# Kernel optimization log

Hardware: AMD Instinct MI355X
Metric: run time of the kernel (lower is better)

Reference implementation:

```python
import jax, jax.numpy as jnp
import numpy as np

N_HEAD, D_K = 8, 16

def _ln(x, g, b):
    m = jnp.mean(x, -1, keepdims=True)
    v = jnp.var(x, -1, keepdims=True)
    return (x - m) * jax.lax.rsqrt(v + 1e-5) * g + b

def _enc_layer(x, wq, bq, wk, bk, wv, bv, wo, bo, g1, be1, cw1, cb1, cw2, cb2, g2, be2):
    B, L, D = x.shape
    q = (x @ wq + bq).reshape(B, L, N_HEAD, D_K)
    k = (x @ wk + bk).reshape(B, L, N_HEAD, D_K)
    v = (x @ wv + bv).reshape(B, L, N_HEAD, D_K)
    attn = jnp.einsum('blhd,bmhd->bhlm', q, k) / jnp.sqrt(jnp.float32(D_K))
    attn = jax.nn.softmax(attn, axis=-1)
    o = jnp.einsum('bhlm,bmhd->blhd', attn, v).reshape(B, L, -1)
    x = _ln(o @ wo + bo + x, g1, be1)          # post-LN residual (MHA)
    h = jax.nn.relu(x @ cw1 + cb1)             # 1x1 conv == linear
    return _ln(h @ cw2 + cb2 + x, g2, be2)     # post-LN residual (FFN)

def setup_inputs() -> dict:
    key = jax.random.key(0)
    ks = jax.random.split(key, 20)
    N, D, NNZ = 100000, 128, 2000000
    B, L, NL, DI = 32, 256, 2, 512
    s = 0.02
    inp = {}
    inp['ego'] = jax.random.normal(ks[0], (N, D), jnp.float32)
    inp['vals'] = jax.random.uniform(ks[1], (NNZ,), jnp.float32) / 20.0  # ~normalized adj values
    inp['W1'] = jax.random.normal(ks[2], (D, D), jnp.float32) * s
    inp['b1'] = jnp.zeros((D,), jnp.float32)
    inp['W2'] = jax.random.normal(ks[3], (D, D), jnp.float32) * s
    inp['b2'] = jnp.zeros((D,), jnp.float32)
    inp['enc_in'] = jax.random.normal(ks[4], (B, L, D), jnp.float32)
    inp['wq'] = jax.random.normal(ks[5], (NL, D, D), jnp.float32) * s
    inp['bq'] = jnp.zeros((NL, D), jnp.float32)
    inp['wk'] = jax.random.normal(ks[6], (NL, D, D), jnp.float32) * s
    inp['bk'] = jnp.zeros((NL, D), jnp.float32)
    inp['wv'] = jax.random.normal(ks[7], (NL, D, D), jnp.float32) * s
    inp['bv'] = jnp.zeros((NL, D), jnp.float32)
    inp['wo'] = jax.random.normal(ks[8], (NL, D, D), jnp.float32) * s
    inp['bo'] = jnp.zeros((NL, D), jnp.float32)
    inp['ln1_g'] = jnp.ones((NL, D), jnp.float32)
    inp['ln1_b'] = jnp.zeros((NL, D), jnp.float32)
    inp['cw1'] = jax.random.normal(ks[9], (NL, D, DI), jnp.float32) * s
    inp['cb1'] = jnp.zeros((NL, DI), jnp.float32)
    inp['cw2'] = jax.random.normal(ks[10], (NL, DI, D), jnp.float32) * s
    inp['cb2'] = jnp.zeros((NL, D), jnp.float32)
    inp['ln2_g'] = jnp.ones((NL, D), jnp.float32)
    inp['ln2_b'] = jnp.zeros((NL, D), jnp.float32)
    inp['rows'] = jnp.sort(jax.random.randint(ks[11], (NNZ,), 0, N, jnp.int32))
    inp['cols'] = jax.random.randint(ks[12], (NNZ,), 0, N, jnp.int32)
    return inp

def reference(ego, vals, W1, b1, W2, b2, enc_in, wq, bq, wk, bk, wv, bv, wo, bo,
              ln1_g, ln1_b, cw1, cb1, cw2, cb2, ln2_g, ln2_b, rows, cols):
    N = ego.shape[0]
    # sparse A_in @ ego  (COO SpMM via gather + segment_sum)
    side = jax.ops.segment_sum(vals[:, None] * ego[cols], rows, num_segments=N)
    # bi-interaction aggregator (dropout=identity in eval)
    sum_emb = jax.nn.leaky_relu((ego + side) @ W1 + b1)
    bi_emb = jax.nn.leaky_relu((ego * side) @ W2 + b2)
    agg = sum_emb + bi_emb
    # transformer encoder over edge sequences
    x = enc_in
    for i in range(wq.shape[0]):
        x = _enc_layer(x, wq[i], bq[i], wk[i], bk[i], wv[i], bv[i], wo[i], bo[i],
                       ln1_g[i], ln1_b[i], cw1[i], cb1[i], cw2[i], cb2[i], ln2_g[i], ln2_b[i])
    return (agg, x)
```

## Files before the change

### kernel.cpp

```cpp
#include <hip/hip_runtime.h>

typedef __attribute__((ext_vector_type(8))) short bf16x8;
typedef __attribute__((ext_vector_type(4))) float f32x4;

__device__ __forceinline__ unsigned short f2b(float f) {
    union { float f; unsigned int i; } u; u.f = f;
    return (unsigned short)((u.i + 0x7FFFu + ((u.i >> 16) & 1u)) >> 16);
}
__device__ __forceinline__ unsigned int packbf2(float a, float b) {
    return (unsigned int)f2b(a) | ((unsigned int)f2b(b) << 16);
}

__device__ __forceinline__ void spmm_block(
    const unsigned int* __restrict__ egob, const float* __restrict__ vals,
    const int* __restrict__ rows, const int* __restrict__ cols,
    float* __restrict__ side, int nnz, int blk)
{
    int tid = threadIdx.x;
    int wave = tid >> 6, lane = tid & 63;
    int e0 = blk * 256 + wave * 64;
    if (e0 >= nnz) return;

    int idx = e0 + lane;
    int last = nnz - 1;
    bool ok = idx < nnz;
    int safe = ok ? idx : last;
    int my_row = rows[safe];
    int my_col = cols[safe];
    float my_val = ok ? vals[safe] : 0.f;

    unsigned int pre[16];
    #pragma unroll
    for (int j = 0; j < 16; ++j) {
        unsigned int c = (unsigned int)__builtin_amdgcn_readlane(my_col, j);
        pre[j] = *(egob + ((size_t)c << 6) + lane);
    }

    float ax = 0.f, ay = 0.f;
    int cur = __builtin_amdgcn_readlane(my_row, 0);
    #pragma unroll
    for (int e = 0; e < 64; ++e) {
        int r = __builtin_amdgcn_readlane(my_row, e);
        float vv = __int_as_float(__builtin_amdgcn_readlane(__float_as_int(my_val), e));
        unsigned int u = pre[e & 15];
        if (e < 48) {
            unsigned int c = (unsigned int)__builtin_amdgcn_readlane(my_col, e + 16);
            pre[e & 15] = *(egob + ((size_t)c << 6) + lane);
        }
        if (r != cur) {
            atomicAdd(&side[(size_t)cur * 128 + lane * 2], ax);
            atomicAdd(&side[(size_t)cur * 128 + lane * 2 + 1], ay);
            ax = 0.f; ay = 0.f; cur = r;
        }
        ax = fmaf(vv, __uint_as_float(u << 16), ax);
        ay = fmaf(vv, __uint_as_float(u & 0xFFFF0000u), ay);
    }
    atomicAdd(&side[(size_t)cur * 128 + lane * 2], ax);
    atomicAdd(&side[(size_t)cur * 128 + lane * 2 + 1], ay);
}

#define LDAB 40
#define LDBI 72
#define LDKV 16

__device__ __forceinline__ void gemm2_core(
    const float* __restrict__ A, const float* __restrict__ W,
    const float* __restrict__ bias, const float* __restrict__ R,
    const float* __restrict__ g, const float* __restrict__ bta,
    float* __restrict__ C, int M, int N, int K, int act,
    int bm, int bn, unsigned short* As, unsigned short* Bs,
    float* redS, float* redSS)
{
    int tid = threadIdx.x, wave = tid >> 6, lane = tid & 63;
    int lm = lane & 15, quad = lane >> 4;
    int wm = wave >> 1, wn = wave & 1;

    f32x4 acc[2][4];
    #pragma unroll
    for (int i = 0; i < 2; ++i)
        #pragma unroll
        for (int j = 0; j < 4; ++j) acc[i][j] = (f32x4)(0.f);

    for (int k0 = 0; k0 < K; k0 += 32) {
        {
            int m = tid >> 2, kc = (tid & 3) * 8;
            const float* p = A + (size_t)(bm + m) * K + k0 + kc;
            float4 a0 = *(const float4*)p, a1 = *(const float4*)(p + 4);
            uint4 pk;
            pk.x = packbf2(a0.x, a0.y); pk.y = packbf2(a0.z, a0.w);
            pk.z = packbf2(a1.x, a1.y); pk.w = packbf2(a1.z, a1.w);
            *(uint4*)&As[m * LDAB + kc] = pk;
        }
        {
            int nn = tid & 127, kh = (tid >> 7) * 16;
            const float* p = W + (size_t)(k0 + kh) * N + bn + nn;
            float w[16];
            #pragma unroll
            for (int j = 0; j < 16; ++j) w[j] = p[(size_t)j * N];
            uint4 pk;
            pk.x = packbf2(w[0], w[1]);  pk.y = packbf2(w[2], w[3]);
            pk.z = packbf2(w[4], w[5]);  pk.w = packbf2(w[6], w[7]);
            *(uint4*)&Bs[nn * LDAB + kh] = pk;
            pk.x = packbf2(w[8], w[9]);  pk.y = packbf2(w[10], w[11]);
            pk.z = packbf2(w[12], w[13]); pk.w = packbf2(w[14], w[15]);
            *(uint4*)&Bs[nn * LDAB + kh + 8] = pk;
        }
        __syncthreads();
        bf16x8 af[2], bfr[4];
        #pragma unroll
        for (int mi = 0; mi < 2; ++mi)
            af[mi] = *(bf16x8*)&As[(wm * 32 + mi * 16 + lm) * LDAB + quad * 8];
        #pragma unroll
        for (int ni = 0; ni < 4; ++ni)
            bfr[ni] = *(bf16x8*)&Bs[(wn * 64 + ni * 16 + lm) * LDAB + quad * 8];
        #pragma unroll
        for (int mi = 0; mi < 2; ++mi)
            #pragma unroll
            for (int ni = 0; ni < 4; ++ni)
                acc[mi][ni] = __builtin_amdgcn_mfma_f32_16x16x32_bf16(
                    af[mi], bfr[ni], acc[mi][ni], 0, 0, 0);
        __syncthreads();
    }

    #pragma unroll
    for (int mi = 0; mi < 2; ++mi) {
        #pragma unroll
        for (int r = 0; r < 4; ++r) {
            int row = bm + wm * 32 + mi * 16 + quad * 4 + r;
            #pragma unroll
            for (int ni = 0; ni < 4; ++ni) {
                int col = bn + wn * 64 + ni * 16 + lm;
                float v = acc[mi][ni][r] + bias[col];
                if (R) v += R[(size_t)row * N + col];
                if (act) v = fmaxf(v, 0.f);
                acc[mi][ni][r] = v;
            }
        }
    }

    if (g) {
        #pragma unroll
        for (int mi = 0; mi < 2; ++mi) {
            #pragma unroll
            for (int r = 0; r < 4; ++r) {
                float s = 0.f, ss = 0.f;
                #pragma unroll
                for (int ni = 0; ni < 4; ++ni) {
                    float v = acc[mi][ni][r];
                    s += v; ss = fmaf(v, v, ss);
                }
                #pragma unroll
                for (int off = 1; off < 16; off <<= 1) {
                    s  += __shfl_xor(s, off, 64);
                    ss += __shfl_xor(ss, off, 64);
                }
                if (lm == 0) {
                    int lr = wm * 32 + mi * 16 + quad * 4 + r;
                    redS[wn * 64 + lr] = s;
                    redSS[wn * 64 + lr] = ss;
                }
            }
        }
        __syncthreads();
        #pragma unroll
        for (int mi = 0; mi < 2; ++mi) {
            #pragma unroll
            for (int r = 0; r < 4; ++r) {
                int lr = wm * 32 + mi * 16 + quad * 4 + r;
                int row = bm + lr;
                float s = redS[lr] + redS[64 + lr];
                float ss = redSS[lr] + redSS[64 + lr];
                float mean = s * (1.f / 128.f);
                float var = ss * (1.f / 128.f) - mean * mean;
                float rstd = rsqrtf(var + 1e-5f);
                #pragma unroll
                for (int ni = 0; ni < 4; ++ni) {
                    int col = wn * 64 + ni * 16 + lm;
                    float y = (acc[mi][ni][r] - mean) * rstd * g[col] + bta[col];
                    C[(size_t)row * 128 + col] = y;
                }
            }
        }
    } else {
        #pragma unroll
        for (int mi = 0; mi < 2; ++mi) {
            #pragma unroll
            for (int r = 0; r < 4; ++r) {
                int row = bm + wm * 32 + mi * 16 + quad * 4 + r;
                #pragma unroll
                for (int ni = 0; ni < 4; ++ni) {
                    int col = bn + wn * 64 + ni * 16 + lm;
                    C[(size_t)row * N + col] = acc[mi][ni][r];
                }
            }
        }
    }
}

__device__ __forceinline__ void bi_core3(
    const float* __restrict__ ego, const float* __restrict__ side,
    const unsigned short* __restrict__ W1t, const unsigned short* __restrict__ W2t,
    const float* __restrict__ b1, const float* __restrict__ b2,
    float* __restrict__ out, int M, int bm,
    unsigned short* Us, unsigned short* Ms)
{
    int tid = threadIdx.x, wave = tid >> 6, lane = tid & 63;
    int lm = lane & 15, quad = lane >> 4;
    int wm = wave >> 1, wn = wave & 1;

    f32x4 acc1[2][4], acc2[2][4];
    #pragma unroll
    for (int i = 0; i < 2; ++i)
        #pragma unroll
        for (int j = 0; j < 4; ++j) { acc1[i][j] = (f32x4)(0.f); acc2[i][j] = (f32x4)(0.f); }

    #pragma unroll
    for (int h = 0; h < 2; ++h) {
        int k0 = h * 64;
        if (h) __syncthreads();
        {
            int m = tid >> 2, kc = (tid & 3) * 16;
            int gm = bm + m;
            float e[16], s[16];
            if (gm < M) {
                const float* pe = ego + (size_t)gm * 128 + k0 + kc;
                const float* ps = side + (size_t)gm * 128 + k0 + kc;
                #pragma unroll
                for (int j = 0; j < 4; ++j) {
                    float4 ev = *(const float4*)(pe + j * 4);
                    float4 sv = *(const float4*)(ps + j * 4);
                    e[j*4+0] = ev.x; e[j*4+1] = ev.y; e[j*4+2] = ev.z; e[j*4+3] = ev.w;
                    s[j*4+0] = sv.x; s[j*4+1] = sv.y; s[j*4+2] = sv.z; s[j*4+3] = sv.w;
                }
            } else {
                #pragma unroll
                for (int j = 0; j < 16; ++j) { e[j] = 0.f; s[j] = 0.f; }
            }
            #pragma unroll
            for (int j = 0; j < 2; ++j) {
                int b0 = j * 8;
                uint4 pu, pv;
                pu.x = packbf2(e[b0+0]+s[b0+0], e[b0+1]+s[b0+1]);
                pu.y = packbf2(e[b0+2]+s[b0+2], e[b0+3]+s[b0+3]);
                pu.z = packbf2(e[b0+4]+s[b0+4], e[b0+5]+s[b0+5]);
                pu.w = packbf2(e[b0+6]+s[b0+6], e[b0+7]+s[b0+7]);
                pv.x = packbf2(e[b0+0]*s[b0+0], e[b0+1]*s[b0+1]);
                pv.y = packbf2(e[b0+2]*s[b0+2], e[b0+3]*s[b0+3]);
                pv.z = packbf2(e[b0+4]*s[b0+4], e[b0+5]*s[b0+5]);
                pv.w = packbf2(e[b0+6]*s[b0+6], e[b0+7]*s[b0+7]);
                *(uint4*)&Us[m * LDBI + kc + b0] = pu;
                *(uint4*)&Ms[m * LDBI + kc + b0] = pv;
            }
        }
        __syncthreads();
        #pragma unroll
        for (int ks = 0; ks < 2; ++ks) {
            bf16x8 au[2], am[2], bf1[4], bf2[4];
            #pragma unroll
            for (int mi = 0; mi < 2; ++mi) {
                int off = (wm * 32 + mi * 16 + lm) * LDBI + ks * 32 + quad * 8;
                au[mi] = *(bf16x8*)&Us[off];
                am[mi] = *(bf16x8*)&Ms[off];
            }
            #pragma unroll
            for (int ni = 0; ni < 4; ++ni) {
                size_t n = (size_t)(wn * 64 + ni * 16 + lm);
                size_t koff = n * 128 + k0 + ks * 32 + quad * 8;
                bf1[ni] = *(const bf16x8*)(W1t + koff);
                bf2[ni] = *(const bf16x8*)(W2t + koff);
            }
            #pragma unroll
            for (int mi = 0; mi < 2; ++mi)
                #pragma unroll
                for (int ni = 0; ni < 4; ++ni) {
                    acc1[mi][ni] = __builtin_amdgcn_mfma_f32_16x16x32_bf16(
                        au[mi], bf1[ni], acc1[mi][ni], 0, 0, 0);
                    acc2[mi][ni] = __builtin_amdgcn_mfma_f32_16x16x32_bf16(
                        am[mi], bf2[ni], acc2[mi][ni], 0, 0, 0);
                }
        }
    }
    #pragma unroll
    for (int mi = 0; mi < 2; ++mi) {
        #pragma unroll
        for (int r = 0; r < 4; ++r) {
            int row = bm + wm * 32 + mi * 16 + quad * 4 + r;
            if (row < M) {
                #pragma unroll
                for (int ni = 0; ni < 4; ++ni) {
                    int col = wn * 64 + ni * 16 + lm;
                    float v1 = acc1[mi][ni][r] + b1[col];
                    v1 = v1 > 0.f ? v1 : 0.01f * v1;
                    float v2 = acc2[mi][ni][r] + b2[col];
                    v2 = v2 > 0.f ? v2 : 0.01f * v2;
                    out[(size_t)row * 128 + col] = v1 + v2;
                }
            }
        }
    }
}

__device__ __forceinline__ void attn_block(
    const float* __restrict__ q, const float* __restrict__ k,
    const float* __restrict__ v, float* __restrict__ o, int NH,
    int blk, float* Ks, float* Vs)
{
    const int L = 256, DK = 16;
    int bh = blk >> 2, qq = blk & 3;
    int b = bh / NH, h = bh % NH;
    int tid = threadIdx.x;
    int qi = tid >> 2, seg = tid & 3;

    int lq = qq * 64 + qi;
    size_t qbase = ((size_t)(b * L + lq) * NH + h) * DK;
    float qr[16];
    #pragma unroll
    for (int d4 = 0; d4 < 4; ++d4) {
        float4 t = *(const float4*)(q + qbase + d4 * 4);
        qr[d4*4+0] = t.x * 0.25f; qr[d4*4+1] = t.y * 0.25f;
        qr[d4*4+2] = t.z * 0.25f; qr[d4*4+3] = t.w * 0.25f;
    }
    float acc[16];
    #pragma unroll
    for (int d = 0; d < 16; ++d) acc[d] = 0.f;
    float mmax = -1e30f, ssum = 0.f;

    for (int c0 = 0; c0 < L; c0 += 128) {
        __syncthreads();
        for (int i = tid; i < 128 * 4; i += 256) {
            int ll = i >> 2, d4 = (i & 3) * 4;
            size_t gg = ((size_t)(b * L + c0 + ll) * NH + h) * DK + d4;
            *(float4*)&Ks[ll * LDKV + d4] = *(const float4*)(k + gg);
            *(float4*)&Vs[ll * LDKV + d4] = *(const float4*)(v + gg);
        }
        __syncthreads();

        for (int i = 0; i < 32; ++i) {
            int kk = (i << 2) | seg;
            const float* kr = &Ks[kk * LDKV];
            float dot = 0.f;
            #pragma unroll
            for (int d4 = 0; d4 < 4; ++d4) {
                float4 kv = *(const float4*)&kr[d4 * 4];
                dot = fmaf(qr[d4*4+0], kv.x, dot);
                dot = fmaf(qr[d4*4+1], kv.y, dot);
                dot = fmaf(qr[d4*4+2], kv.z, dot);
                dot = fmaf(qr[d4*4+3], kv.w, dot);
            }
            if (dot > mmax) {
                float alpha = __expf(mmax - dot);
                ssum *= alpha;
                #pragma unroll
                for (int d = 0; d < 16; ++d) acc[d] *= alpha;
                mmax = dot;
            }
            float p = __expf(dot - mmax);
            ssum += p;
            const float* vr = &Vs[kk * LDKV];
            #pragma unroll
            for (int d4 = 0; d4 < 4; ++d4) {
                float4 vv = *(const float4*)&vr[d4 * 4];
                acc[d4*4+0] = fmaf(p, vv.x, acc[d4*4+0]);
                acc[d4*4+1] = fmaf(p, vv.y, acc[d4*4+1]);
                acc[d4*4+2] = fmaf(p, vv.z, acc[d4*4+2]);
                acc[d4*4+3] = fmaf(p, vv.w, acc[d4*4+3]);
            }
        }
    }

    float m1 = fmaxf(mmax, __shfl_xor(mmax, 1, 64));
    float m2 = fmaxf(m1, __shfl_xor(m1, 2, 64));
    float f = __expf(mmax - m2);
    float sl = ssum * f;
    sl += __shfl_xor(sl, 1, 64);
    sl += __shfl_xor(sl, 2, 64);
    #pragma unroll
    for (int d = 0; d < 16; ++d) {
        float a = acc[d] * f;
        a += __shfl_xor(a, 1, 64);
        a += __shfl_xor(a, 2, 64);
        acc[d] = a;
    }
    if (seg == 0) {
        float inv = 1.f / sl;
        #pragma unroll
        for (int d4 = 0; d4 < 4; ++d4) {
            float4 t;
            t.x = acc[d4*4+0] * inv; t.y = acc[d4*4+1] * inv;
            t.z = acc[d4*4+2] * inv; t.w = acc[d4*4+3] * inv;
            *(float4*)(o + qbase + d4 * 4) = t;
        }
    }
}


__global__ __launch_bounds__(256) void qkv2_pre(
    const float* __restrict__ A,
    const float* __restrict__ wq, const float* __restrict__ wk, const float* __restrict__ wv,
    const float* __restrict__ bq, const float* __restrict__ bk, const float* __restrict__ bv,
    float* __restrict__ Q, float* __restrict__ Ko, float* __restrict__ V, int M, int encGy,
    float* __restrict__ side, int Nn,
    const float* __restrict__ ego, unsigned int* __restrict__ egob,
    const float* __restrict__ W1, const float* __restrict__ W2,
    unsigned short* __restrict__ W1t, unsigned short* __restrict__ W2t,
    int encN, int ZB, int CB, int WTB)
{
    __shared__ unsigned short As[64 * LDAB];
    __shared__ unsigned short Bs[128 * LDAB];
    __shared__ float redS[128], redSS[128];
    int gid = blockIdx.x;
    int tid = threadIdx.x;
    if (gid >= encN) {
        int j = gid - encN;
        if (j < ZB) {
            size_t n4 = (size_t)Nn * 32;
            float4 z = make_float4(0.f, 0.f, 0.f, 0.f);
            for (size_t i = (size_t)j * 256 + tid; i < n4; i += (size_t)ZB * 256)
                ((float4*)side)[i] = z;
        } else if (j < ZB + CB) {
            int c = j - ZB;
            size_t n4 = (size_t)Nn * 32;
            for (size_t i = (size_t)c * 256 + tid; i < n4; i += (size_t)CB * 256) {
                float4 a = *(const float4*)(ego + i * 4);
                uint2 p;
                p.x = packbf2(a.x, a.y);
                p.y = packbf2(a.z, a.w);
                *(uint2*)(egob + i * 2) = p;
            }
        } else {
            int c = j - ZB - CB;
            for (int ch = c * 256 + tid; ch < 4096; ch += WTB * 256) {
                int w = ch >> 11, rem = ch & 2047;
                int n = rem >> 4, k8 = rem & 15;
                const float* src = w ? W2 : W1;
                unsigned short* dst = w ? W2t : W1t;
                float t[8];
                #pragma unroll
                for (int jj = 0; jj < 8; ++jj)
                    t[jj] = src[(size_t)(k8 * 8 + jj) * 128 + n];
                uint4 pk;
                pk.x = packbf2(t[0], t[1]); pk.y = packbf2(t[2], t[3]);
                pk.z = packbf2(t[4], t[5]); pk.w = packbf2(t[6], t[7]);
                *(uint4*)&dst[(size_t)n * 128 + k8 * 8] = pk;
            }
        }
        return;
    }
    int sel = gid / encGy, by = gid % encGy;
    const float* W = (sel == 0) ? wq : (sel == 1) ? wk : wv;
    const float* b = (sel == 0) ? bq : (sel == 1) ? bk : bv;
    float* C = (sel == 0) ? Q : (sel == 1) ? Ko : V;
    gemm2_core(A, W, b, nullptr, nullptr, nullptr, C, M, 128, 128, 0,
               by * 64, 0, As, Bs, redS, redSS);
}

__global__ __launch_bounds__(256) void qkv2_spmm(
    const float* __restrict__ A,
    const float* __restrict__ wq, const float* __restrict__ wk, const float* __restrict__ wv,
    const float* __restrict__ bq, const float* __restrict__ bk, const float* __restrict__ bv,
    float* __restrict__ Q, float* __restrict__ Ko, float* __restrict__ V, int M, int encGy,
    const unsigned int* __restrict__ egob, const float* __restrict__ vals,
    const int* __restrict__ rows, const int* __restrict__ cols,
    float* __restrict__ side, int nnz, int spmmBase, int encN)
{
    __shared__ unsigned short As[64 * LDAB];
    __shared__ unsigned short Bs[128 * LDAB];
    __shared__ float redS[128], redSS[128];
    int gid = blockIdx.x;
    if (gid >= encN) {
        spmm_block(egob, vals, rows, cols, side, nnz, spmmBase + gid - encN);
        return;
    }
    int sel = gid / encGy, by = gid % encGy;
    const float* W = (sel == 0) ? wq : (sel == 1) ? wk : wv;
    const float* b = (sel == 0) ? bq : (sel == 1) ? bk : bv;
    float* C = (sel == 0) ? Q : (sel == 1) ? Ko : V;
    gemm2_core(A, W, b, nullptr, nullptr, nullptr, C, M, 128, 128, 0,
               by * 64, 0, As, Bs, redS, redSS);
}

__global__ __launch_bounds__(256) void gemm2_spmm(
    const float* __restrict__ A, const float* __restrict__ W,
    const float* __restrict__ bias, const float* __restrict__ R,
    const float* __restrict__ g, const float* __restrict__ bta,
    float* __restrict__ C, int M, int N, int K, int act, int encGy,
    const unsigned int* __restrict__ egob, const float* __restrict__ vals,
    const int* __restrict__ rows, const int* __restrict__ cols,
    float* __restrict__ side, int nnz, int spmmBase, int encN)
{
    __shared__ unsigned short As[64 * LDAB];
    __shared__ unsigned short Bs[128 * LDAB];
    __shared__ float redS[128], redSS[128];
    int gid = blockIdx.x;
    if (gid >= encN) {
        spmm_block(egob, vals, rows, cols, side, nnz, spmmBase + gid - encN);
        return;
    }
    int bx = gid / encGy, by = gid % encGy;
    gemm2_core(A, W, bias, R, g, bta, C, M, N, K, act,
               by * 64, bx * 128, As, Bs, redS, redSS);
}

__global__ __launch_bounds__(256) void gemm2_bi3(
    const float* __restrict__ A, const float* __restrict__ W,
    const float* __restrict__ bias, const float* __restrict__ R,
    const float* __restrict__ g, const float* __restrict__ bta,
    float* __restrict__ C, int M, int N, int K, int act, int encGy, int encN,
    const float* __restrict__ ego, const float* __restrict__ side,
    const unsigned short* __restrict__ W1t, const unsigned short* __restrict__ W2t,
    const float* __restrict__ b1, const float* __restrict__ b2,
    float* __restrict__ out, int Mbi, int biBase)
{
    __shared__ char smem[18432];
    int gid = blockIdx.x;
    if (gid < encN) {
        unsigned short* As = (unsigned short*)smem;
        unsigned short* Bs = (unsigned short*)(smem + 5120);
        float* redS  = (float*)(smem + 15360);
        float* redSS = (float*)(smem + 15360 + 512);
        int bx = gid / encGy, by = gid % encGy;
        gemm2_core(A, W, bias, R, g, bta, C, M, N, K, act,
                   by * 64, bx * 128, As, Bs, redS, redSS);
    } else {
        int bb = biBase + (gid - encN);
        unsigned short* Us = (unsigned short*)smem;
        unsigned short* Ms = (unsigned short*)(smem + 9216);
        bi_core3(ego, side, W1t, W2t, b1, b2, out, Mbi, bb * 64, Us, Ms);
    }
}

__global__ __launch_bounds__(256) void attn_spmm(
    const float* __restrict__ q, const float* __restrict__ k,
    const float* __restrict__ v, float* __restrict__ o, int NH,
    const unsigned int* __restrict__ egob, const float* __restrict__ vals,
    const int* __restrict__ rows, const int* __restrict__ cols,
    float* __restrict__ side, int nnz, int spmmBase, int encN)
{
    __shared__ float Ks[128 * LDKV];
    __shared__ float Vs[128 * LDKV];
    int gid = blockIdx.x;
    if (gid >= encN) {
        spmm_block(egob, vals, rows, cols, side, nnz, spmmBase + gid - encN);
        return;
    }
    attn_block(q, k, v, o, NH, gid, Ks, Vs);
}

extern "C" void kernel_launch(void* const* d_in, const int* in_sizes, int n_in,
                              void* d_out, int out_size, void* d_ws, size_t ws_size,
                              hipStream_t stream) {
    const float* ego    = (const float*)d_in[0];
    const float* vals   = (const float*)d_in[1];
    const float* W1     = (const float*)d_in[2];
    const float* b1     = (const float*)d_in[3];
    const float* W2     = (const float*)d_in[4];
    const float* b2     = (const float*)d_in[5];
    const float* enc_in = (const float*)d_in[6];
    const float* wq  = (const float*)d_in[7];
    const float* bq  = (const float*)d_in[8];
    const float* wk  = (const float*)d_in[9];
    const float* bk  = (const float*)d_in[10];
    const float* wv  = (const float*)d_in[11];
    const float* bv  = (const float*)d_in[12];
    const float* wo  = (const float*)d_in[13];
    const float* bo  = (const float*)d_in[14];
    const float* ln1_g = (const float*)d_in[15];
    const float* ln1_b = (const float*)d_in[16];
    const float* cw1 = (const float*)d_in[17];
    const float* cb1 = (const float*)d_in[18];
    const float* cw2 = (const float*)d_in[19];
    const float* cb2 = (const float*)d_in[20];
    const float* ln2_g = (const float*)d_in[21];
    const float* ln2_b = (const float*)d_in[22];
    const int* rows = (const int*)d_in[23];
    const int* cols = (const int*)d_in[24];

    const int D = 128, DI = 512, NH = 8, L = 256;
    const int Nn   = in_sizes[0] / D;
    const int nnz  = in_sizes[1];
    const int NL   = in_sizes[7] / (D * D);
    const int Menc = in_sizes[6] / D;
    const int Bb   = Menc / L;

    float* ws = (float*)d_ws;
    size_t off = 0;
    float* side = ws + off; off += (size_t)Nn * D;
    float* Qb = ws + off; off += (size_t)Menc * D;
    float* Kb = ws + off; off += (size_t)Menc * D;
    float* Vb = ws + off; off += (size_t)Menc * D;
    float* Ob = ws + off; off += (size_t)Menc * D;
    float* XA = ws + off; off += (size_t)Menc * D;
    float* XB = ws + off; off += (size_t)Menc * D;
    float* Hb = ws + off; off += (size_t)Menc * DI;
    unsigned int* egob = (unsigned int*)(ws + off); off += (size_t)Nn * (D / 2);
    unsigned short* W1t = (unsigned short*)(ws + off); off += (size_t)D * D / 2;
    unsigned short* W2t = (unsigned short*)(ws + off); off += (size_t)D * D / 2;

    float* outAgg = (float*)d_out;
    float* outX   = (float*)d_out + (size_t)Nn * D;

    const int spmmBlocks = (nnz + 255) / 256;
    const int nSpmmStages = 5 * NL - 3;
    const int perS = (spmmBlocks + nSpmmStages - 1) / nSpmmStages;
    const int biTiles = (Nn + 63) / 64;
    const int perB = (biTiles + 1) / 2;
    const int biStart = 5 * NL - 1;
    const int encGy = Menc / 64;
    const int ZB = 512, CB = 1024, WTB = 16;
    int sidx = 0, sci = 0, bci = 0;

    const float* x = enc_in;
    for (int i = 0; i < NL; ++i) {
        const size_t wOff = (size_t)i * D * D;
        int base, cnt;
        #define SPMM_CHUNK base = sci * perS; cnt = spmmBlocks - base; \
                           if (cnt < 0) cnt = 0; if (cnt > perS) cnt = perS; sci++
        #define BI_CHUNK   base = bci * perB; cnt = biTiles - base; \
                           if (cnt < 0) cnt = 0; if (cnt > perB) cnt = perB; bci++

        sidx++;
        if (sidx == 1) {
            qkv2_pre<<<3 * encGy + ZB + CB + WTB, 256, 0, stream>>>(
                x, wq + wOff, wk + wOff, wv + wOff,
                bq + (size_t)i * D, bk + (size_t)i * D, bv + (size_t)i * D,
                Qb, Kb, Vb, Menc, encGy,
                side, Nn, ego, egob, W1, W2, W1t, W2t, 3 * encGy, ZB, CB, WTB);
        } else {
            SPMM_CHUNK;
            qkv2_spmm<<<3 * encGy + cnt, 256, 0, stream>>>(
                x, wq + wOff, wk + wOff, wv + wOff,
                bq + (size_t)i * D, bk + (size_t)i * D, bv + (size_t)i * D,
                Qb, Kb, Vb, Menc, encGy,
                egob, vals, rows, cols, side, nnz, base, 3 * encGy);
        }

        sidx++;
        SPMM_CHUNK;
        attn_spmm<<<Bb * NH * 4 + cnt, 256, 0, stream>>>(
            Qb, Kb, Vb, Ob, NH,
            egob, vals, rows, cols, side, nnz, base, Bb * NH * 4);

        sidx++;
        SPMM_CHUNK;
        gemm2_spmm<<<encGy + cnt, 256, 0, stream>>>(
            Ob, wo + wOff, bo + (size_t)i * D, x,
            ln1_g + (size_t)i * D, ln1_b + (size_t)i * D, XA, Menc, D, D, 0, encGy,
            egob, vals, rows, cols, side, nnz, base, encGy);

        sidx++;
        if (sidx >= biStart) {
            BI_CHUNK;
            gemm2_bi3<<<4 * encGy + cnt, 256, 0, stream>>>(
                XA, cw1 + (size_t)i * D * DI, cb1 + (size_t)i * DI, nullptr,
                nullptr, nullptr, Hb, Menc, DI, D, 1, encGy, 4 * encGy,
                ego, side, W1t, W2t, b1, b2, outAgg, Nn, base);
        } else {
            SPMM_CHUNK;
            gemm2_spmm<<<4 * encGy + cnt, 256, 0, stream>>>(
                XA, cw1 + (size_t)i * D * DI, cb1 + (size_t)i * DI, nullptr,
                nullptr, nullptr, Hb, Menc, DI, D, 1, encGy,
                egob, vals, rows, cols, side, nnz, base, 4 * encGy);
        }

        sidx++;
        float* dst = (i == NL - 1) ? outX : XB;
        if (sidx >= biStart) {
            BI_CHUNK;
            gemm2_bi3<<<encGy + cnt, 256, 0, stream>>>(
                Hb, cw2 + (size_t)i * DI * D, cb2 + (size_t)i * D, XA,
                ln2_g + (size_t)i * D, ln2_b + (size_t)i * D, dst, Menc, D, DI, 0,
                encGy, encGy,
                ego, side, W1t, W2t, b1, b2, outAgg, Nn, base);
        } else {
            SPMM_CHUNK;
            gemm2_spmm<<<encGy + cnt, 256, 0, stream>>>(
                Hb, cw2 + (size_t)i * DI * D, cb2 + (size_t)i * D, XA,
                ln2_g + (size_t)i * D, ln2_b + (size_t)i * D, dst, Menc, D, DI, 0, encGy,
                egob, vals, rows, cols, side, nnz, base, encGy);
        }
        #undef SPMM_CHUNK
        #undef BI_CHUNK
        x = XB;
    }
}
```

Baseline: 453.1 us.

## Place side-work blocks first in fused grids and stage full K in bi-interaction tile

Every fused kernel now numbers its SpMM, zero/convert and bi-interaction blocks before the encoder GEMM/attention blocks, so the long irregular work is dispatched first and the short dense tiles fill in behind it. The bi-interaction core now stages all 128 K columns of the (ego+side) and (ego*side) bf16 tiles in shared memory at once. That drops the second staging pass and one barrier, but raises shared memory for that kernel from 18 KB to 34 KB, which may lower occupancy for the GEMM blocks sharing it.

After: 500.2 us. 10.4% more time.

```diff
diff --git a/kernel.cpp b/kernel.cpp
--- a/kernel.cpp
+++ b/kernel.cpp
@@ -60,7 +60,7 @@
 }
 
 #define LDAB 40
-#define LDBI 72
+#define LDBI2 136
 #define LDKV 16
 
 __device__ __forceinline__ void gemm2_core(
@@ -197,7 +197,7 @@
     }
 }
 
-__device__ __forceinline__ void bi_core3(
+__device__ __forceinline__ void bi_core4(
     const float* __restrict__ ego, const float* __restrict__ side,
     const unsigned short* __restrict__ W1t, const unsigned short* __restrict__ W2t,
     const float* __restrict__ b1, const float* __restrict__ b2,
@@ -214,71 +214,67 @@
         #pragma unroll
         for (int j = 0; j < 4; ++j) { acc1[i][j] = (f32x4)(0.f); acc2[i][j] = (f32x4)(0.f); }
 
-    #pragma unroll
-    for (int h = 0; h < 2; ++h) {
-        int k0 = h * 64;
-        if (h) __syncthreads();
-        {
-            int m = tid >> 2, kc = (tid & 3) * 16;
-            int gm = bm + m;
-            float e[16], s[16];
-            if (gm < M) {
-                const float* pe = ego + (size_t)gm * 128 + k0 + kc;
-                const float* ps = side + (size_t)gm * 128 + k0 + kc;
-                #pragma unroll
-                for (int j = 0; j < 4; ++j) {
-                    float4 ev = *(const float4*)(pe + j * 4);
-                    float4 sv = *(const float4*)(ps + j * 4);
-                    e[j*4+0] = ev.x; e[j*4+1] = ev.y; e[j*4+2] = ev.z; e[j*4+3] = ev.w;
-                    s[j*4+0] = sv.x; s[j*4+1] = sv.y; s[j*4+2] = sv.z; s[j*4+3] = sv.w;
-                }
-            } else {
-                #pragma unroll
-                for (int j = 0; j < 16; ++j) { e[j] = 0.f; s[j] = 0.f; }
-            }
-            #pragma unroll
-            for (int j = 0; j < 2; ++j) {
-                int b0 = j * 8;
-                uint4 pu, pv;
-                pu.x = packbf2(e[b0+0]+s[b0+0], e[b0+1]+s[b0+1]);
-                pu.y = packbf2(e[b0+2]+s[b0+2], e[b0+3]+s[b0+3]);
-                pu.z = packbf2(e[b0+4]+s[b0+4], e[b0+5]+s[b0+5]);
-                pu.w = packbf2(e[b0+6]+s[b0+6], e[b0+7]+s[b0+7]);
-                pv.x = packbf2(e[b0+0]*s[b0+0], e[b0+1]*s[b0+1]);
-                pv.y = packbf2(e[b0+2]*s[b0+2], e[b0+3]*s[b0+3]);
-                pv.z = packbf2(e[b0+4]*s[b0+4], e[b0+5]*s[b0+5]);
-                pv.w = packbf2(e[b0+6]*s[b0+6], e[b0+7]*s[b0+7]);
-                *(uint4*)&Us[m * LDBI + kc + b0] = pu;
-                *(uint4*)&Ms[m * LDBI + kc + b0] = pv;
-            }
-        }
-        __syncthreads();
-        #pragma unroll
-        for (int ks = 0; ks < 2; ++ks) {
-            bf16x8 au[2], am[2], bf1[4], bf2[4];
-            #pragma unroll
-            for (int mi = 0; mi < 2; ++mi) {
-                int off = (wm * 32 + mi * 16 + lm) * LDBI + ks * 32 + quad * 8;
-                au[mi] = *(bf16x8*)&Us[off];
-                am[mi] = *(bf16x8*)&Ms[off];
-            }
+    {
+        int m = tid >> 2, kc = (tid & 3) * 32;
+        int gm = bm + m;
+        float e[32], s[32];
+        if (gm < M) {
+            const float* pe = ego + (size_t)gm * 128 + kc;
+            const float* ps = side + (size_t)gm * 128 + kc;
+            #pragma unroll
+            for (int j = 0; j < 8; ++j) {
+                float4 ev = *(const float4*)(pe + j * 4);
+                float4 sv = *(const float4*)(ps + j * 4);
+                e[j*4+0] = ev.x; e[j*4+1] = ev.y; e[j*4+2] = ev.z; e[j*4+3] = ev.w;
+                s[j*4+0] = sv.x; s[j*4+1] = sv.y; s[j*4+2] = sv.z; s[j*4+3] = sv.w;
+            }
+        } else {
+            #pragma unroll
+            for (int j = 0; j < 32; ++j) { e[j] = 0.f; s[j] = 0.f; }
+        }
+        #pragma unroll
+        for (int j = 0; j < 4; ++j) {
+            int b0 = j * 8;
+            uint4 pu, pv;
+            pu.x = packbf2(e[b0+0]+s[b0+0], e[b0+1]+s[b0+1]);
+            pu.y = packbf2(e[b0+2]+s[b0+2], e[b0+3]+s[b0+3]);
+            pu.z = packbf2(e[b0+4]+s[b0+4], e[b0+5]+s[b0+5]);
+            pu.w = packbf2(e[b0+6]+s[b0+6], e[b0+7]+s[b0+7]);
+            pv.x = packbf2(e[b0+0]*s[b0+0], e[b0+1]*s[b0+1]);
+            pv.y = packbf2(e[b0+2]*s[b0+2], e[b0+3]*s[b0+3]);
+            pv.z = packbf2(e[b0+4]*s[b0+4], e[b0+5]*s[b0+5]);
+            pv.w = packbf2(e[b0+6]*s[b0+6], e[b0+7]*s[b0+7]);
+            *(uint4*)&Us[m * LDBI2 + kc + b0] = pu;
+            *(uint4*)&Ms[m * LDBI2 + kc + b0] = pv;
+        }
+    }
+    __syncthreads();
+
+    #pragma unroll
+    for (int ks = 0; ks < 4; ++ks) {
+        bf16x8 au[2], am[2], bf1[4], bf2[4];
+        #pragma unroll
+        for (int mi = 0; mi < 2; ++mi) {
+            int off = (wm * 32 + mi * 16 + lm) * LDBI2 + ks * 32 + quad * 8;
+            au[mi] = *(bf16x8*)&Us[off];
+            am[mi] = *(bf16x8*)&Ms[off];
+        }
+        #pragma unroll
+        for (int ni = 0; ni < 4; ++ni) {
+            size_t n = (size_t)(wn * 64 + ni * 16 + lm);
+            size_t koff = n * 128 + ks * 32 + quad * 8;
+            bf1[ni] = *(const bf16x8*)(W1t + koff);
+            bf2[ni] = *(const bf16x8*)(W2t + koff);
+        }
+        #pragma unroll
+        for (int mi = 0; mi < 2; ++mi)
             #pragma unroll
             for (int ni = 0; ni < 4; ++ni) {
-                size_t n = (size_t)(wn * 64 + ni * 16 + lm);
-                size_t koff = n * 128 + k0 + ks * 32 + quad * 8;
-                bf1[ni] = *(const bf16x8*)(W1t + koff);
-                bf2[ni] = *(const bf16x8*)(W2t + koff);
-            }
-            #pragma unroll
-            for (int mi = 0; mi < 2; ++mi)
-                #pragma unroll
-                for (int ni = 0; ni < 4; ++ni) {
-                    acc1[mi][ni] = __builtin_amdgcn_mfma_f32_16x16x32_bf16(
-                        au[mi], bf1[ni], acc1[mi][ni], 0, 0, 0);
-                    acc2[mi][ni] = __builtin_amdgcn_mfma_f32_16x16x32_bf16(
-                        am[mi], bf2[ni], acc2[mi][ni], 0, 0, 0);
-                }
-        }
+                acc1[mi][ni] = __builtin_amdgcn_mfma_f32_16x16x32_bf16(
+                    au[mi], bf1[ni], acc1[mi][ni], 0, 0, 0);
+                acc2[mi][ni] = __builtin_amdgcn_mfma_f32_16x16x32_bf16(
+                    am[mi], bf2[ni], acc2[mi][ni], 0, 0, 0);
+            }
     }
     #pragma unroll
     for (int mi = 0; mi < 2; ++mi) {
@@ -403,15 +399,15 @@
     const float* __restrict__ ego, unsigned int* __restrict__ egob,
     const float* __restrict__ W1, const float* __restrict__ W2,
     unsigned short* __restrict__ W1t, unsigned short* __restrict__ W2t,
-    int encN, int ZB, int CB, int WTB)
+    int ZB, int CB, int WTB)
 {
     __shared__ unsigned short As[64 * LDAB];
     __shared__ unsigned short Bs[128 * LDAB];
     __shared__ float redS[128], redSS[128];
     int gid = blockIdx.x;
     int tid = threadIdx.x;
-    if (gid >= encN) {
-        int j = gid - encN;
+    if (gid < ZB + CB + WTB) {
+        int j = gid;
         if (j < ZB) {
             size_t n4 = (size_t)Nn * 32;
             float4 z = make_float4(0.f, 0.f, 0.f, 0.f);
@@ -446,7 +442,8 @@
         }
         return;
     }
-    int sel = gid / encGy, by = gid % encGy;
+    int egid = gid - (ZB + CB + WTB);
+    int sel = egid / encGy, by = egid % encGy;
     const float* W = (sel == 0) ? wq : (sel == 1) ? wk : wv;
     const float* b = (sel == 0) ? bq : (sel == 1) ? bk : bv;
     float* C = (sel == 0) ? Q : (sel == 1) ? Ko : V;
@@ -461,17 +458,18 @@
     float* __restrict__ Q, float* __restrict__ Ko, float* __restrict__ V, int M, int encGy,
     const unsigned int* __restrict__ egob, const float* __restrict__ vals,
     const int* __restrict__ rows, const int* __restrict__ cols,
-    float* __restrict__ side, int nnz, int spmmBase, int encN)
+    float* __restrict__ side, int nnz, int spmmBase, int sideCnt)
 {
     __shared__ unsigned short As[64 * LDAB];
     __shared__ unsigned short Bs[128 * LDAB];
     __shared__ float redS[128], redSS[128];
     int gid = blockIdx.x;
-    if (gid >= encN) {
-        spmm_block(egob, vals, rows, cols, side, nnz, spmmBase + gid - encN);
+    if (gid < sideCnt) {
+        spmm_block(egob, vals, rows, cols, side, nnz, spmmBase + gid);
         return;
     }
-    int sel = gid / encGy, by = gid % encGy;
+    int egid = gid - sideCnt;
+    int sel = egid / encGy, by = egid % encGy;
     const float* W = (sel == 0) ? wq : (sel == 1) ? wk : wv;
     const float* b = (sel == 0) ? bq : (sel == 1) ? bk : bv;
     float* C = (sel == 0) ? Q : (sel == 1) ? Ko : V;
@@ -486,46 +484,49 @@
     float* __restrict__ C, int M, int N, int K, int act, int encGy,
     const unsigned int* __restrict__ egob, const float* __restrict__ vals,
     const int* __restrict__ rows, const int* __restrict__ cols,
-    float* __restrict__ side, int nnz, int spmmBase, int encN)
+    float* __restrict__ side, int nnz, int spmmBase, int sideCnt)
 {
     __shared__ unsigned short As[64 * LDAB];
     __shared__ unsigned short Bs[128 * LDAB];
     __shared__ float redS[128], redSS[128];
     int gid = blockIdx.x;
-    if (gid >= encN) {
-        spmm_block(egob, vals, rows, cols, side, nnz, spmmBase + gid - encN);
+    if (gid < sideCnt) {
+        spmm_block(egob, vals, rows, cols, side, nnz, spmmBase + gid);
         return;
     }
-    int bx = gid / encGy, by = gid % encGy;
+    int egid = gid - sideCnt;
+    int bx = egid / encGy, by = egid % encGy;
     gemm2_core(A, W, bias, R, g, bta, C, M, N, K, act,
                by * 64, bx * 128, As, Bs, redS, redSS);
 }
 
-__global__ __launch_bounds__(256) void gemm2_bi3(
+__global__ __launch_bounds__(256) void gemm2_bi4(
     const float* __restrict__ A, const float* __restrict__ W,
     const float* __restrict__ bias, const float* __restrict__ R,
     const float* __restrict__ g, const float* __restrict__ bta,
-    float* __restrict__ C, int M, int N, int K, int act, int encGy, int encN,
+    float* __restrict__ C, int M, int N, int K, int act, int encGy,
     const float* __restrict__ ego, const float* __restrict__ side,
     const unsigned short* __restrict__ W1t, const unsigned short* __restrict__ W2t,
     const float* __restrict__ b1, const float* __restrict__ b2,
-    float* __restrict__ out, int Mbi, int biBase)
-{
-    __shared__ char smem[18432];
+    float* __restrict__ out, int Mbi, int biBase, int biCnt)
+{
+    __shared__ uint4 smem4[34816 / 16];
+    char* smem = (char*)smem4;
     int gid = blockIdx.x;
-    if (gid < encN) {
+    if (gid < biCnt) {
+        int bb = biBase + gid;
+        unsigned short* Us = (unsigned short*)smem;
+        unsigned short* Ms = (unsigned short*)(smem + 17408);
+        bi_core4(ego, side, W1t, W2t, b1, b2, out, Mbi, bb * 64, Us, Ms);
+    } else {
+        int egid = gid - biCnt;
         unsigned short* As = (unsigned short*)smem;
         unsigned short* Bs = (unsigned short*)(smem + 5120);
         float* redS  = (float*)(smem + 15360);
         float* redSS = (float*)(smem + 15360 + 512);
-        int bx = gid / encGy, by = gid % encGy;
+        int bx = egid / encGy, by = egid % encGy;
         gemm2_core(A, W, bias, R, g, bta, C, M, N, K, act,
                    by * 64, bx * 128, As, Bs, redS, redSS);
-    } else {
-        int bb = biBase + (gid - encN);
-        unsigned short* Us = (unsigned short*)smem;
-        unsigned short* Ms = (unsigned short*)(smem + 9216);
-        bi_core3(ego, side, W1t, W2t, b1, b2, out, Mbi, bb * 64, Us, Ms);
     }
 }
 
@@ -534,16 +535,16 @@
     const float* __restrict__ v, float* __restrict__ o, int NH,
     const unsigned int* __restrict__ egob, const float* __restrict__ vals,
     const int* __restrict__ rows, const int* __restrict__ cols,
-    float* __restrict__ side, int nnz, int spmmBase, int encN)
+    float* __restrict__ side, int nnz, int spmmBase, int sideCnt)
 {
     __shared__ float Ks[128 * LDKV];
     __shared__ float Vs[128 * LDKV];
     int gid = blockIdx.x;
-    if (gid >= encN) {
-        spmm_block(egob, vals, rows, cols, side, nnz, spmmBase + gid - encN);
+    if (gid < sideCnt) {
+        spmm_block(egob, vals, rows, cols, side, nnz, spmmBase + gid);
         return;
     }
-    attn_block(q, k, v, o, NH, gid, Ks, Vs);
+    attn_block(q, k, v, o, NH, gid - sideCnt, Ks, Vs);
 }
 
 extern "C" void kernel_launch(void* const* d_in, const int* in_sizes, int n_in,
@@ -624,59 +625,58 @@
                 x, wq + wOff, wk + wOff, wv + wOff,
                 bq + (size_t)i * D, bk + (size_t)i * D, bv + (size_t)i * D,
                 Qb, Kb, Vb, Menc, encGy,
-                side, Nn, ego, egob, W1, W2, W1t, W2t, 3 * encGy, ZB, CB, WTB);
+                side, Nn, ego, egob, W1, W2, W1t, W2t, ZB, CB, WTB);
         } else {
             SPMM_CHUNK;
             qkv2_spmm<<<3 * encGy + cnt, 256, 0, stream>>>(
                 x, wq + wOff, wk + wOff, wv + wOff,
                 bq + (size_t)i * D, bk + (size_t)i * D, bv + (size_t)i * D,
                 Qb, Kb, Vb, Menc, encGy,
-                egob, vals, rows, cols, side, nnz, base, 3 * encGy);
+                egob, vals, rows, cols, side, nnz, base, cnt);
         }
 
         sidx++;
         SPMM_CHUNK;
         attn_spmm<<<Bb * NH * 4 + cnt, 256, 0, stream>>>(
             Qb, Kb, Vb, Ob, NH,
-            egob, vals, rows, cols, side, nnz, base, Bb * NH * 4);
+            egob, vals, rows, cols, side, nnz, base, cnt);
 
         sidx++;
         SPMM_CHUNK;
         gemm2_spmm<<<encGy + cnt, 256, 0, stream>>>(
             Ob, wo + wOff, bo + (size_t)i * D, x,
             ln1_g + (size_t)i * D, ln1_b + (size_t)i * D, XA, Menc, D, D, 0, encGy,
-            egob, vals, rows, cols, side, nnz, base, encGy);
+            egob, vals, rows, cols, side, nnz, base, cnt);
 
         sidx++;
         if (sidx >= biStart) {
             BI_CHUNK;
-            gemm2_bi3<<<4 * encGy + cnt, 256, 0, stream>>>(
+            gemm2_bi4<<<4 * encGy + cnt, 256, 0, stream>>>(
                 XA, cw1 + (size_t)i * D * DI, cb1 + (size_t)i * DI, nullptr,
-                nullptr, nullptr, Hb, Menc, DI, D, 1, encGy, 4 * encGy,
-                ego, side, W1t, W2t, b1, b2, outAgg, Nn, base);
+                nullptr, nullptr, Hb, Menc, DI, D, 1, encGy,
+                ego, side, W1t, W2t, b1, b2, outAgg, Nn, base, cnt);
         } else {
             SPMM_CHUNK;
             gemm2_spmm<<<4 * encGy + cnt, 256, 0, stream>>>(
                 XA, cw1 + (size_t)i * D * DI, cb1 + (size_t)i * DI, nullptr,
                 nullptr, nullptr, Hb, Menc, DI, D, 1, encGy,
-                egob, vals, rows, cols, side, nnz, base, 4 * encGy);
+                egob, vals, rows, cols, side, nnz, base, cnt);
         }
 
         sidx++;
         float* dst = (i == NL - 1) ? outX : XB;
         if (sidx >= biStart) {
             BI_CHUNK;
-            gemm2_bi3<<<encGy + cnt, 256, 0, stream>>>(
+            gemm2_bi4<<<encGy + cnt, 256, 0, stream>>>(
                 Hb, cw2 + (size_t)i * DI * D, cb2 + (size_t)i * D, XA,
-                ln2_g + (size_t)i * D, ln2_b + (size_t)i * D, dst, Menc, D, DI, 0,
-                encGy, encGy,
-                ego, side, W1t, W2t, b1, b2, outAgg, Nn, base);
+                ln2_g + (size_t)i * D, ln2_b + (size_t)i * D, dst, Menc, D, DI, 0, encGy,
+                ego, side, W1t, W2t, b1, b2, outAgg, Nn, base, cnt);
         } else {
             SPMM_CHUNK;
             gemm2_spmm<<<encGy + cnt, 256, 0, stream>>>(
                 Hb, cw2 + (size_t)i * DI * D, cb2 + (size_t)i * D, XA,
                 ln2_g + (size_t)i * D, ln2_b + (size_t)i * D, dst, Menc, D, DI, 0, encGy,
-                egob, vals, rows, cols, side, nnz, base, encGy);
+                egob, vals, rows, cols, side, nnz, base, cnt);
         }
         #undef SPMM_CHUNK
         #undef BI_CHUNK
```
